# Performance work log

Measured on AMD Instinct MI355X. Metric: run time of the kernel, lower is better.

The kernel has to match this reference:

```python
import jax, jax.numpy as jnp
import numpy as np

V, D, B, L = 8000, 256, 64, 64
CONCENTRATION = 5.0  # config['model']['args']['concentrator_factor']
GAW = 0.5            # initial value of _lambda parameter
EPS_COS = 1e-8       # torch cosine_similarity eps


def setup_inputs() -> dict:
    key = jax.random.key(0)
    ks = jax.random.split(key, 8)
    concepts_list = jax.random.randint(ks[0], (B, L), 0, V)
    concepts_length = jax.random.randint(ks[1], (B,), 0, L)
    contrastive_mask = jax.random.randint(ks[2], (B, V), 0, 2).astype(jnp.int32)
    # raw edge matrix, then row-range normalization as in init_params
    edge_raw = jax.random.uniform(ks[3], (V, V), dtype=jnp.float32)
    rng = (edge_raw.max(axis=1) - edge_raw.min(axis=1))[:, None]
    edge_matrix = edge_raw / (rng + (rng == 0).astype(jnp.float32))
    affectiveness = jax.random.uniform(ks[4], (V,), dtype=jnp.float32)
    embed_w = jax.random.normal(ks[5], (V, D), dtype=jnp.float32)
    embed_kb_w = jax.random.normal(ks[6], (V, D), dtype=jnp.float32)
    lam = jnp.full((V,), GAW, dtype=jnp.float32)
    return {
        "concepts_list": concepts_list,
        "concepts_length": concepts_length,
        "contrastive_mask": contrastive_mask,
        "edge_matrix": edge_matrix,
        "affectiveness": affectiveness,
        "embed_w": embed_w,
        "embed_kb_w": embed_kb_w,
        "lam": lam,
    }


def reference(concepts_list, concepts_length, contrastive_mask,
              edge_matrix, affectiveness, embed_w, embed_kb_w, lam):
    # [B, L, D] concept token embeddings
    concepts_embedded = embed_w[concepts_list]
    # valid-prefix mask per row: positions < concepts_length[i]
    pos_mask = (jnp.arange(L)[None, :] < concepts_length[:, None])  # [B, L] bool
    denom = jnp.maximum(concepts_length, 1).astype(concepts_embedded.dtype)[:, None]
    # per-row masked mean (rows with length 0 -> zeros, matching empty_tensor)
    row_mean = (concepts_embedded * pos_mask[..., None]).sum(axis=1) / denom  # [B, D]
    context_representation = row_mean.mean(axis=0)  # [D]
    # |cosine similarity| between context and every KB embedding -> [V]
    ctx_norm = jnp.linalg.norm(context_representation)
    kb_norms = jnp.linalg.norm(embed_kb_w, axis=1)
    cosine_similarity = jnp.abs(
        (embed_kb_w @ context_representation) / jnp.maximum(kb_norms * ctx_norm, EPS_COS)
    )
    # [B, L, V] local graph rows for each concept token
    local_graph = edge_matrix[concepts_list]
    rel = local_graph * cosine_similarity          # broadcast over V
    aff = (local_graph > 0).astype(local_graph.dtype) * affectiveness
    concepts_weights = lam * rel + (1.0 - lam) * aff  # [B, L, V]
    concepts_weights = jnp.where(contrastive_mask[:, None, :] == 0, 1e-9, concepts_weights)
    attn = jax.nn.softmax(concepts_weights * CONCENTRATION, axis=2)  # [B, L, V]
    concepts_embedding = jnp.einsum('blv,vd->bld', attn, embed_kb_w)  # [B, L, D]
    # masked mean over valid prefix (length 0 -> zeros)
    concepts_embedding = (concepts_embedding * pos_mask[..., None]).sum(axis=1) / denom  # [B, D]
    local_nodes = jnp.broadcast_to(embed_kb_w[None], (B, V, D))
    return concepts_embedding, local_nodes
```

## Files before the change

### kernel.cpp

```cpp
#include <hip/hip_runtime.h>
#include <cstddef>
#include <cstdint>
#include <cmath>

#define V 8000
#define D 256
#define B 64
#define L 64
#define SPLIT 4
#define NCH 200
#define VC 40
#define ROW4 (V * D / 4)

#define PART_OFF 0
#define CTX_OFF  16384
#define W1_OFF   16640
#define W0_OFF   24640
#define A_OFF    32640
#define P_OFF    544640

typedef float f32x4 __attribute__((ext_vector_type(4)));

__global__ __launch_bounds__(256) void k1_ctx(const int* __restrict__ clist,
                                              const int* __restrict__ clen,
                                              const float* __restrict__ embw,
                                              float* __restrict__ part) {
    int b = blockIdx.x, d = threadIdx.x;
    __shared__ int cl[L];
    if (d < L) cl[d] = clist[b * L + d];
    __syncthreads();
    int len = clen[b];
    int nl = len < L ? len : L;
    float a0 = 0.f, a1 = 0.f, a2 = 0.f, a3 = 0.f;
    int l = 0;
    for (; l + 4 <= nl; l += 4) {
        a0 += embw[(size_t)cl[l]     * D + d];
        a1 += embw[(size_t)cl[l + 1] * D + d];
        a2 += embw[(size_t)cl[l + 2] * D + d];
        a3 += embw[(size_t)cl[l + 3] * D + d];
    }
    for (; l < nl; ++l) a0 += embw[(size_t)cl[l] * D + d];
    float denom = (float)(len < 1 ? 1 : len);
    part[b * D + d] = (a0 + a1 + a2 + a3) / denom;
}

__global__ void k1b_reduce(const float* __restrict__ part, float* __restrict__ ctx) {
    int d = threadIdx.x;
    float s = 0.f;
    #pragma unroll 8
    for (int b = 0; b < B; ++b) s += part[b * D + d];
    ctx[d] = s * (1.0f / (float)B);
}

__global__ __launch_bounds__(256) void k2_cos(const float* __restrict__ kb,
                                              const float* __restrict__ lam,
                                              const float* __restrict__ aff,
                                              const float* __restrict__ ctx,
                                              float* __restrict__ w1,
                                              float* __restrict__ w0,
                                              float* __restrict__ A) {
    int tid = threadIdx.x;
    int gtid = blockIdx.x * 256 + tid;
    A[gtid] = 0.f;

    __shared__ float ctxs[D];
    __shared__ float red[5];
    int wid = tid >> 6, lane = tid & 63;
    float c = ctx[tid];
    ctxs[tid] = c;
    float sq = c * c;
    #pragma unroll
    for (int o = 32; o > 0; o >>= 1) sq += __shfl_xor(sq, o);
    if (lane == 0) red[wid] = sq;
    __syncthreads();
    if (tid == 0) red[4] = sqrtf(red[0] + red[1] + red[2] + red[3]);
    __syncthreads();
    float ctxnorm = red[4];

    int v = blockIdx.x * 4 + wid;
    float4 k4 = *(const float4*)(kb + (size_t)v * D + lane * 4);
    float4 c4 = *(const float4*)(ctxs + lane * 4);
    float dot = k4.x * c4.x + k4.y * c4.y + k4.z * c4.z + k4.w * c4.w;
    float sqs = k4.x * k4.x + k4.y * k4.y + k4.z * k4.z + k4.w * k4.w;
    #pragma unroll
    for (int o = 32; o > 0; o >>= 1) {
        dot += __shfl_xor(dot, o);
        sqs += __shfl_xor(sqs, o);
    }
    if (lane == 0) {
        float cosv = fabsf(dot) / fmaxf(sqrtf(sqs) * ctxnorm, 1e-8f);
        float la = lam[v];
        w1[v] = 5.0f * la * cosv;
        w0[v] = 5.0f * (1.0f - la) * aff[v];
    }
}

__global__ __launch_bounds__(1024) void k3_softmax(
    const int* __restrict__ clist, const int* __restrict__ clen,
    const int* __restrict__ cmask, const float* __restrict__ edge,
    const float* __restrict__ w1g, const float* __restrict__ w0g,
    float* __restrict__ A) {
    int b = blockIdx.x, split = blockIdx.y;
    int tid = threadIdx.x;
    int wid = tid >> 6, lane = tid & 63;
    bool active = tid < (V / 8);
    int v0 = tid * 8;
    __shared__ float lsum[2][16];

    float w1r[8], w0r[8], acc[8];
    int mr[8];
    if (active) {
        float4 t0 = *(const float4*)(w1g + v0);
        float4 t1 = *(const float4*)(w1g + v0 + 4);
        w1r[0]=t0.x; w1r[1]=t0.y; w1r[2]=t0.z; w1r[3]=t0.w;
        w1r[4]=t1.x; w1r[5]=t1.y; w1r[6]=t1.z; w1r[7]=t1.w;
        t0 = *(const float4*)(w0g + v0);
        t1 = *(const float4*)(w0g + v0 + 4);
        w0r[0]=t0.x; w0r[1]=t0.y; w0r[2]=t0.z; w0r[3]=t0.w;
        w0r[4]=t1.x; w0r[5]=t1.y; w0r[6]=t1.z; w0r[7]=t1.w;
        int4 m0 = *(const int4*)(cmask + (size_t)b * V + v0);
        int4 m1 = *(const int4*)(cmask + (size_t)b * V + v0 + 4);
        mr[0]=m0.x; mr[1]=m0.y; mr[2]=m0.z; mr[3]=m0.w;
        mr[4]=m1.x; mr[5]=m1.y; mr[6]=m1.z; mr[7]=m1.w;
    }
    #pragma unroll
    for (int j = 0; j < 8; ++j) acc[j] = 0.f;

    int len = clen[b];
    int nl = len < L ? len : L;
    int parity = 0;
    for (int l = split; l < nl; l += SPLIT) {
        int c = clist[b * L + l];
        const float* er = edge + (size_t)c * V;
        float p[8];
        float s = 0.f;
        if (active) {
            float4 e0 = *(const float4*)(er + v0);
            float4 e1 = *(const float4*)(er + v0 + 4);
            float ev[8] = {e0.x, e0.y, e0.z, e0.w, e1.x, e1.y, e1.z, e1.w};
            #pragma unroll
            for (int j = 0; j < 8; ++j) {
                float e = ev[j];
                float wv = w1r[j] * e + (e > 0.f ? w0r[j] : 0.f);
                wv = (mr[j] != 0) ? wv : 5e-9f;
                p[j] = __expf(wv);
                s += p[j];
            }
        } else {
            #pragma unroll
            for (int j = 0; j < 8; ++j) p[j] = 0.f;
        }
        #pragma unroll
        for (int o = 32; o > 0; o >>= 1) s += __shfl_xor(s, o);
        if (lane == 0) lsum[parity][wid] = s;
        __syncthreads();
        float tot = 0.f;
        #pragma unroll
        for (int k = 0; k < 16; ++k) tot += lsum[parity][k];
        float inv = 1.0f / tot;
        if (active) {
            #pragma unroll
            for (int j = 0; j < 8; ++j) acc[j] += p[j] * inv;
        }
        parity ^= 1;
    }
    if (active) {
        #pragma unroll
        for (int j = 0; j < 8; ++j)
            atomicAdd(&A[(size_t)b * V + v0 + j], acc[j]);
    }
}

__global__ __launch_bounds__(256) void k4_gemv(const float* __restrict__ A,
                                               const float* __restrict__ kb,
                                               float* __restrict__ P) {
    int ch = blockIdx.x;
    int tid = threadIdx.x;
    int vbase = ch * VC;
    __shared__ float Al[B][VC];
    for (int i = tid; i < B * VC; i += 256) {
        int bt = i / VC, vl = i % VC;
        Al[bt][vl] = A[(size_t)bt * V + vbase + vl];
    }
    __syncthreads();
    float acc[B];
    #pragma unroll
    for (int t = 0; t < B; ++t) acc[t] = 0.f;
    for (int vl = 0; vl < VC; ++vl) {
        float kv = kb[(size_t)(vbase + vl) * D + tid];
        #pragma unroll
        for (int t = 0; t < B; ++t) acc[t] += Al[t][vl] * kv;
    }
    #pragma unroll
    for (int t = 0; t < B; ++t)
        P[(size_t)ch * (B * D) + (size_t)t * D + tid] = acc[t];
}

__global__ void k5_out0(const float* __restrict__ P, const int* __restrict__ clen,
                        float* __restrict__ out0) {
    int b = blockIdx.x, d = threadIdx.x;
    float s = 0.f;
    #pragma unroll 8
    for (int ch = 0; ch < NCH; ++ch) s += P[(size_t)ch * (B * D) + b * D + d];
    int len = clen[b];
    out0[b * D + d] = s / (float)(len < 1 ? 1 : len);
}

__global__ __launch_bounds__(256) void k6_bcast(const f32x4* __restrict__ kb4,
                                                f32x4* __restrict__ out4) {
    int idx = blockIdx.x * 256 + threadIdx.x;
    f32x4 f = kb4[idx];
    int bstart = blockIdx.x & (B - 1);
    #pragma unroll
    for (int bb = 0; bb < B; ++bb) {
        int b = (bb + bstart) & (B - 1);
        __builtin_nontemporal_store(f, &out4[(size_t)b * ROW4 + idx]);
    }
}

extern "C" void kernel_launch(void* const* d_in, const int* in_sizes, int n_in,
                              void* d_out, int out_size, void* d_ws, size_t ws_size,
                              hipStream_t stream) {
    const int*   clist = (const int*)d_in[0];
    const int*   clen  = (const int*)d_in[1];
    const int*   cmask = (const int*)d_in[2];
    const float* edge  = (const float*)d_in[3];
    const float* aff   = (const float*)d_in[4];
    const float* embw  = (const float*)d_in[5];
    const float* kb    = (const float*)d_in[6];
    const float* lam   = (const float*)d_in[7];
    float* out0 = (float*)d_out;
    float* out1 = out0 + B * D;
    float* ws   = (float*)d_ws;

    k1_ctx<<<dim3(B), dim3(256), 0, stream>>>(clist, clen, embw, ws + PART_OFF);
    k1b_reduce<<<dim3(1), dim3(D), 0, stream>>>(ws + PART_OFF, ws + CTX_OFF);
    k2_cos<<<dim3(V / 4), dim3(256), 0, stream>>>(kb, lam, aff, ws + CTX_OFF,
                                                  ws + W1_OFF, ws + W0_OFF, ws + A_OFF);
    k3_softmax<<<dim3(B, SPLIT), dim3(1024), 0, stream>>>(clist, clen, cmask, edge,
                                                          ws + W1_OFF, ws + W0_OFF, ws + A_OFF);
    k4_gemv<<<dim3(NCH), dim3(256), 0, stream>>>(ws + A_OFF, kb, ws + P_OFF);
    k5_out0<<<dim3(B), dim3(D), 0, stream>>>(ws + P_OFF, clen, out0);
    k6_bcast<<<dim3(ROW4 / 256), dim3(256), 0, stream>>>((const f32x4*)kb,
                                                         (f32x4*)out1);
}
```

Baseline: 268.8 us.

## Fuse context reduction into cosine kernel and gemv reduction via atomics

The separate single-block context reduction kernel is removed, and every k2_cos block now reduces the 64 per-row partial means itself. The k5 output-reduction kernel is also removed. k4_gemv scales its partial sums by 1/len and atomically adds them into out0, which k2_cos now zeroes. This cuts two launches and the 13MB partial buffer traffic, at the cost of redundant partial reads in every k2 block, atomic contention on out0, and a non-deterministic summation order.

```diff
diff --git a/kernel.cpp b/kernel.cpp
--- a/kernel.cpp
+++ b/kernel.cpp
@@ -13,11 +13,9 @@
 #define ROW4 (V * D / 4)
 
 #define PART_OFF 0
-#define CTX_OFF  16384
-#define W1_OFF   16640
-#define W0_OFF   24640
-#define A_OFF    32640
-#define P_OFF    544640
+#define W1_OFF   16384
+#define W0_OFF   24384
+#define A_OFF    32384
 
 typedef float f32x4 __attribute__((ext_vector_type(4)));
 
@@ -44,30 +42,28 @@
     part[b * D + d] = (a0 + a1 + a2 + a3) / denom;
 }
 
-__global__ void k1b_reduce(const float* __restrict__ part, float* __restrict__ ctx) {
-    int d = threadIdx.x;
-    float s = 0.f;
-    #pragma unroll 8
-    for (int b = 0; b < B; ++b) s += part[b * D + d];
-    ctx[d] = s * (1.0f / (float)B);
-}
-
 __global__ __launch_bounds__(256) void k2_cos(const float* __restrict__ kb,
                                               const float* __restrict__ lam,
                                               const float* __restrict__ aff,
-                                              const float* __restrict__ ctx,
+                                              const float* __restrict__ part,
                                               float* __restrict__ w1,
                                               float* __restrict__ w0,
-                                              float* __restrict__ A) {
+                                              float* __restrict__ A,
+                                              float* __restrict__ out0) {
     int tid = threadIdx.x;
     int gtid = blockIdx.x * 256 + tid;
     A[gtid] = 0.f;
+    if (gtid < B * D) out0[gtid] = 0.f;
 
     __shared__ float ctxs[D];
     __shared__ float red[5];
+    float s = 0.f;
+    #pragma unroll 8
+    for (int b = 0; b < B; ++b) s += part[b * D + tid];
+    float c = s * (1.0f / (float)B);
+    ctxs[tid] = c;
+
     int wid = tid >> 6, lane = tid & 63;
-    float c = ctx[tid];
-    ctxs[tid] = c;
     float sq = c * c;
     #pragma unroll
     for (int o = 32; o > 0; o >>= 1) sq += __shfl_xor(sq, o);
@@ -173,11 +169,17 @@
 
 __global__ __launch_bounds__(256) void k4_gemv(const float* __restrict__ A,
                                                const float* __restrict__ kb,
-                                               float* __restrict__ P) {
+                                               const int* __restrict__ clen,
+                                               float* __restrict__ out0) {
     int ch = blockIdx.x;
     int tid = threadIdx.x;
     int vbase = ch * VC;
     __shared__ float Al[B][VC];
+    __shared__ float inv[B];
+    if (tid < B) {
+        int len = clen[tid];
+        inv[tid] = 1.0f / (float)(len < 1 ? 1 : len);
+    }
     for (int i = tid; i < B * VC; i += 256) {
         int bt = i / VC, vl = i % VC;
         Al[bt][vl] = A[(size_t)bt * V + vbase + vl];
@@ -193,17 +195,7 @@
     }
     #pragma unroll
     for (int t = 0; t < B; ++t)
-        P[(size_t)ch * (B * D) + (size_t)t * D + tid] = acc[t];
-}
-
-__global__ void k5_out0(const float* __restrict__ P, const int* __restrict__ clen,
-                        float* __restrict__ out0) {
-    int b = blockIdx.x, d = threadIdx.x;
-    float s = 0.f;
-    #pragma unroll 8
-    for (int ch = 0; ch < NCH; ++ch) s += P[(size_t)ch * (B * D) + b * D + d];
-    int len = clen[b];
-    out0[b * D + d] = s / (float)(len < 1 ? 1 : len);
+        atomicAdd(&out0[t * D + tid], acc[t] * inv[t]);
 }
 
 __global__ __launch_bounds__(256) void k6_bcast(const f32x4* __restrict__ kb4,
@@ -234,13 +226,12 @@
     float* ws   = (float*)d_ws;
 
     k1_ctx<<<dim3(B), dim3(256), 0, stream>>>(clist, clen, embw, ws + PART_OFF);
-    k1b_reduce<<<dim3(1), dim3(D), 0, stream>>>(ws + PART_OFF, ws + CTX_OFF);
-    k2_cos<<<dim3(V / 4), dim3(256), 0, stream>>>(kb, lam, aff, ws + CTX_OFF,
-                                                  ws + W1_OFF, ws + W0_OFF, ws + A_OFF);
+    k2_cos<<<dim3(V / 4), dim3(256), 0, stream>>>(kb, lam, aff, ws + PART_OFF,
+                                                  ws + W1_OFF, ws + W0_OFF,
+                                                  ws + A_OFF, out0);
     k3_softmax<<<dim3(B, SPLIT), dim3(1024), 0, stream>>>(clist, clen, cmask, edge,
                                                           ws + W1_OFF, ws + W0_OFF, ws + A_OFF);
-    k4_gemv<<<dim3(NCH), dim3(256), 0, stream>>>(ws + A_OFF, kb, ws + P_OFF);
-    k5_out0<<<dim3(B), dim3(D), 0, stream>>>(ws + P_OFF, clen, out0);
+    k4_gemv<<<dim3(NCH), dim3(256), 0, stream>>>(ws + A_OFF, kb, clen, out0);
     k6_bcast<<<dim3(ROW4 / 256), dim3(256), 0, stream>>>((const f32x4*)kb,
                                                          (f32x4*)out1);
 }
```

Result: faster. 257.1 us (-4.3%).
